# Optimization experiments

Measured on AMD Instinct MI355X. Metric: run time of the kernel, lower is better.

Reference implementation:

```python
import jax, jax.numpy as jnp
import numpy as np
from jax import lax

NEG = -1e30  # log-space 'zero' that stays finite for stable grads

T, B, V, L = 2000, 64, 128, 100


def ctc_cost(acts, labels2d, sizes, label_lens):
    """warp-ctc style CTC: acts are raw logits (T,B,V), blank index 0.
    Returns summed negative log-likelihood over the batch, shape (1,)."""
    Tn, Bn, Vn = acts.shape
    Ln = labels2d.shape[1]
    S = 2 * Ln + 1  # extended label length: blank,l1,blank,l2,...,blank
    lp = jax.nn.log_softmax(acts, axis=-1)  # (T,B,V)

    # extended label sequence per example: even positions blank(0), odd = labels
    ext = jnp.zeros((Bn, S), dtype=labels2d.dtype).at[:, 1::2].set(labels2d)
    # skip (s-2 -> s) allowed iff ext[s] != blank and ext[s] != ext[s-2]
    prev2 = jnp.concatenate([jnp.full((Bn, 2), -1, ext.dtype), ext[:, :-2]], axis=1)
    can_skip = (ext != 0) & (ext != prev2)  # (B,S)

    # gather per-state emission log-probs for all timesteps: (T,B,S)
    lp_ext = jnp.take_along_axis(lp, jnp.broadcast_to(ext[None], (Tn, Bn, S)), axis=2)

    # alpha init at t=0: states 0 (blank) and 1 (first label)
    alpha0 = (jnp.full((Bn, S), NEG, lp.dtype)
              .at[:, 0].set(lp_ext[0, :, 0])
              .at[:, 1].set(lp_ext[0, :, 1]))

    # per-timestep activity mask: freeze alpha once t >= sizes[b]
    active = jnp.arange(1, Tn)[:, None] < sizes[None, :]  # (T-1, B)

    def step(alpha, x):
        lp_t, act = x  # (B,S), (B,)
        a1 = jnp.concatenate([jnp.full((Bn, 1), NEG, alpha.dtype), alpha[:, :-1]], axis=1)
        a2 = jnp.concatenate([jnp.full((Bn, 2), NEG, alpha.dtype), alpha[:, :-2]], axis=1)
        a2 = jnp.where(can_skip, a2, NEG)
        new = jnp.logaddexp(jnp.logaddexp(alpha, a1), a2) + lp_t
        alpha = jnp.where(act[:, None], new, alpha)
        return alpha, None

    alpha, _ = lax.scan(step, alpha0, (lp_ext[1:], active))

    # log-likelihood ends at extended states S_b-1 (final blank) and S_b-2 (final label)
    S_b = 2 * label_lens + 1
    last = jnp.take_along_axis(alpha, (S_b - 1)[:, None], axis=1)[:, 0]
    last2 = jnp.take_along_axis(alpha, (S_b - 2)[:, None], axis=1)[:, 0]
    ll = jnp.logaddexp(last, last2)  # (B,)
    return -jnp.sum(ll)[None]  # shape (1,) like the torch module


def setup_inputs() -> dict:
    key = jax.random.key(0)
    k1, k2, k3 = jax.random.split(key, 3)
    inp = jax.random.normal(k1, (T, B, V), dtype=jnp.float32)
    # labels in [1, V): 0 is reserved for blank
    target = jax.random.randint(k2, (B * L,), 1, V, dtype=jnp.int32)
    # frame counts in [T//2, T], always >= 2L+1 so every path is feasible
    sizes = jax.random.randint(k3, (B,), T // 2, T + 1, dtype=jnp.int32)
    label_lens = jnp.full((B,), L, dtype=jnp.int32)
    return {"input": inp, "target": target, "sizes": sizes, "label_lens": label_lens}


def reference(input, target, sizes, label_lens):
    labels2d = target.reshape(sizes.shape[0], -1)  # all label_lens equal -> clean reshape
    return ctc_cost(input, labels2d, sizes, label_lens)
```

## Files before the change

kernel.cpp:

```cpp
#include <hip/hip_runtime.h>


#define TT 2000
#define BB 64
#define VV 128
#define LL 100
#define RECW 56
#define REC_BASE 256
#define NEGF (-1e30f)
#define L2E 1.44269504f
#define LN2 0.69314718f

__device__ __forceinline__ float wave_max64(float v) {
#pragma unroll
  for (int o = 32; o > 0; o >>= 1) v = fmaxf(v, __shfl_xor(v, o, 64));
  return v;
}
__device__ __forceinline__ float wave_sum64(float v) {
#pragma unroll
  for (int o = 32; o > 0; o >>= 1) v += __shfl_xor(v, o, 64);
  return v;
}
__device__ __forceinline__ float blo(unsigned u) { return __uint_as_float(u << 16); }
__device__ __forceinline__ float bhi(unsigned u) { return __uint_as_float(u & 0xFFFF0000u); }
__device__ __forceinline__ unsigned b16(float x) {
  unsigned b = __float_as_uint(x);
  return (b + 0x7FFFu + ((b >> 16) & 1u)) >> 16;
}

__global__ __launch_bounds__(256) void k_gather(const float* __restrict__ acts,
                                                const int* __restrict__ target,
                                                float* __restrict__ ws) {
  const int lane = threadIdx.x & 63;
  const int w = threadIdx.x >> 6;
  const int r = blockIdx.x * 4 + w;
  if (r >= TT * BB) return;
  const int b = r % BB;
  const int t = r / BB;
  const float* row = acts + (size_t)r * VV;
  float x0 = row[lane];
  float x1 = row[lane + 64];
  float m = wave_max64(fmaxf(x0, x1));
  float e = __builtin_exp2f((x0 - m) * L2E) + __builtin_exp2f((x1 - m) * L2E);
  float s = wave_sum64(e);
  float lse = m + __builtin_log2f(s) * LN2;
  const int* lab = target + b * LL;
  const int j = lane;
  int ilo = (2 * j < 100) ? 2 * j : 99;
  int ihi = (2 * j + 1 < 100) ? 2 * j + 1 : 99;
  int cl = lab[ilo], ch = lab[ihi];
  float ya = __shfl(x0, cl & 63, 64), yb = __shfl(x1, cl & 63, 64);
  float ylo = (cl < 64) ? ya : yb;
  float yc = __shfl(x0, ch & 63, 64), yd = __shfl(x1, ch & 63, 64);
  float yhi = (ch < 64) ? yc : yd;
  float glo = (j < 50) ? (ylo - lse) : NEGF;
  float ghi = (j < 50) ? (yhi - lse) : NEGF;
  float gb = __shfl(x0, 0, 64) - lse;
  float gm = wave_max64(fmaxf(fmaxf(glo, ghi), gb));
  float qlo = __builtin_exp2f((glo - gm) * L2E);
  float qhi = __builtin_exp2f((ghi - gm) * L2E);
  unsigned u = b16(qlo) | (b16(qhi) << 16);
  unsigned* rec = (unsigned*)(ws + REC_BASE + ((size_t)b * TT + t) * RECW);
  if (j < 50) rec[2 + j] = u;
  if (j == 50) rec[52] = 0u;
  if (j == 0) {
    ((float*)rec)[0] = __builtin_exp2f((gb - gm) * L2E);
    ((float*)rec)[1] = gm;
  }
}

#define BPER __builtin_amdgcn_ds_bpermute
#define CL50(x) ((x) < 0 ? 0 : ((x) > 50 ? 50 : (x)))

#define DECLR(P) float2 P##h0, P##h1, P##h2, P##h3; \
                 unsigned P##b0, P##b1, P##b2, P##b3, P##c0, P##c1, P##c2, P##c3, P##uA

#define PREF(P, bidx) do {                                                   \
  int bi_ = (bidx); bi_ = (bi_ < bcap) ? bi_ : bcap; if (bi_ < 0) bi_ = 0;   \
  const float* r0_ = recs_b + (size_t)(tA + TS * 4 * bi_) * RECW;            \
  P##h0 = *(const float2*)(r0_);                                             \
  P##h1 = *(const float2*)(r0_ + TS * RECW);                                 \
  P##h2 = *(const float2*)(r0_ + TS * 2 * RECW);                             \
  P##h3 = *(const float2*)(r0_ + TS * 3 * RECW);                             \
  P##b0 = ((const unsigned*)r0_)[pbofs];                                     \
  P##c0 = ((const unsigned*)r0_)[pcofs];                                     \
  P##b1 = ((const unsigned*)(r0_ + TS * RECW))[pbofs];                       \
  P##c1 = ((const unsigned*)(r0_ + TS * RECW))[pcofs];                       \
  P##b2 = ((const unsigned*)(r0_ + TS * 2 * RECW))[pbofs];                   \
  P##c2 = ((const unsigned*)(r0_ + TS * 2 * RECW))[pcofs];                   \
  P##b3 = ((const unsigned*)(r0_ + TS * 3 * RECW))[pbofs];                   \
  P##c3 = ((const unsigned*)(r0_ + TS * 3 * RECW))[pcofs];                   \
  P##uA = ((const unsigned*)r0_)[payofs];                                    \
} while (0)

#define STEP(qbv, gmv, cx, cy, bx, by, ay, NH) do {                          \
  const float qb_ = (qbv); msum += (gmv);                                    \
  o3 = __builtin_fmaf(cs_o3, o1, o3 + o2) * (cy);                            \
  o2 = (o2 + o1) * qb_;                                                      \
  o1 = __builtin_fmaf(cs_o1, h1, o1 + o0) * (cx);                            \
  o0 = (o0 + h1) * qb_;                                                      \
  if (NH >= 1) { h1 = __builtin_fmaf(cs_h1, h3, h1 + h2) * (by);             \
                 h2 = (h2 + h3) * qb_; }                                     \
  if (NH >= 2) { h3 = __builtin_fmaf(cs_h3, h5, h3 + h4) * (bx);             \
                 h4 = (h4 + h5) * qb_; }                                     \
  if (NH >= 3) { h5 = __builtin_fmaf(cs_h5, h7, h5 + h6) * (ay);             \
                 h6 = (h6 + h7) * qb_; }                                     \
} while (0)

#define UQ(P, K, QV) float4 QV; do {                                         \
  if constexpr (DIR) {                                                       \
    QV = (float4){bhi(P##b##K), blo(P##b##K),                                \
                  bhi(P##c##K) * cmask, blo(P##c##K) * cmask};               \
  } else {                                                                   \
    QV = (float4){blo(P##b##K), bhi(P##b##K), blo(P##c##K), bhi(P##c##K)};   \
  }                                                                          \
} while (0)

#define COMPA(P) do {                                                        \
  UQ(P, 0, q0_); UQ(P, 1, q1_); UQ(P, 2, q2_); UQ(P, 3, q3_);                \
  float aYv = DIR ? blo(P##uA) : bhi(P##uA);                                 \
  STEP(P##h0.x, P##h0.y, q0_.z, q0_.w, q0_.x, q0_.y, aYv, 3);                \
  STEP(P##h1.x, P##h1.y, q1_.z, q1_.w, q1_.x, q1_.y, 0.f, 2);                \
  STEP(P##h2.x, P##h2.y, q2_.z, q2_.w, q2_.x, q2_.y, 0.f, 1);                \
  STEP(P##h3.x, P##h3.y, q3_.z, q3_.w, 0.f, 0.f, 0.f, 0);                    \
  unsigned p01_ = b16(o0) | (b16(o1) << 16);                                 \
  unsigned p23_ = b16(o2) | (b16(o3) << 16);                                 \
  *(uint2*)(exbU + 2 * l) = (uint2){p01_, p23_};                             \
  exbU[128 + l] = (unsigned)offs;                                            \
} while (0)

#define FINL() do {                                                          \
  asm volatile("" ::: "memory");                                             \
  uint2 W1_ = *(const uint2*)(exbU + 2 * ((l >= 1) ? (l - 1) : 0));          \
  uint2 W2_ = *(const uint2*)(exbU + 2 * ((l >= 2) ? (l - 2) : 0));          \
  int ro1_ = (int)exbU[128 + ((l >= 1) ? (l - 1) : 0)];                      \
  int ro2_ = (int)exbU[128 + ((l >= 2) ? (l - 2) : 0)];                      \
  ro1_ = (l >= 1) ? ro1_ : -(1 << 29);                                       \
  ro2_ = (l >= 2) ? ro2_ : -(1 << 29);                                       \
  float m_ = fmaxf(fmaxf(o0, o1), fmaxf(o2, o3));                            \
  int eb_ = (int)((__float_as_uint(m_) >> 23) & 255u);                       \
  int t1_ = offs + (eb_ ? (eb_ - 127) : -126);                               \
  int mx_ = (ro1_ > ro2_) ? ro1_ : ro2_;                                     \
  int onew_ = (t1_ > mx_) ? t1_ : mx_;                                       \
  int ds_ = offs - onew_;  ds_ = (ds_ < -300) ? -300 : ds_;                  \
  int d1_ = ro1_ - onew_, d2_ = ro2_ - onew_;                                \
  d1_ = (d1_ < -300) ? -300 : d1_;                                           \
  d2_ = (d2_ < -300) ? -300 : d2_;                                           \
  o0 = ldexpf(o0, ds_); o1 = ldexpf(o1, ds_);                                \
  o2 = ldexpf(o2, ds_); o3 = ldexpf(o3, ds_);                                \
  h1 = ldexpf(bhi(W1_.y), d1_);                                              \
  h2 = ldexpf(blo(W1_.y), d1_);                                              \
  h3 = ldexpf(bhi(W1_.x), d1_);                                              \
  h4 = ldexpf(blo(W1_.x), d1_);                                              \
  h5 = ldexpf(bhi(W2_.y), d2_);                                              \
  h6 = ldexpf(blo(W2_.y), d2_);                                              \
  h7 = ldexpf(bhi(W2_.x), d2_);                                              \
  offs = onew_;                                                              \
} while (0)

template <int DIR>
__device__ __forceinline__ void run_chain(const int* __restrict__ target,
                                          const int* __restrict__ lablens,
                                          const float* __restrict__ recs_b,
                                          float* exb, int size, int b, int l) {
  unsigned* exbU = (unsigned*)exb;
  const int mid = (size - 1) >> 1;
  const int sizeP = DIR ? (size - 1 - mid) : (mid + 1);
  const int* lab = target + b * LL;
  const int lc = (l < 50) ? l : 50;
  const int tA = DIR ? (size - 2) : 1;
  constexpr int TS = DIR ? -1 : 1;
  const int bcap = DIR ? ((size - 5) >> 2) : 498;
  const int pbofs = 2 + (DIR ? CL50(50 - l) : CL50(l - 1));
  const int pcofs = 2 + (DIR ? CL50(49 - l) : CL50(l));
  const int payofs = 2 + (DIR ? CL50(51 - l) : CL50(l - 2));
  const float cmask = (l < 50) ? 1.f : 0.f;
  const int idx1 = ((l + 63) & 63) << 2;
  const float msk1 = (4 * l - 1 >= 0) ? 1.f : 0.f;
  int i0, i1, i2, i3, i4, i5;
  if constexpr (DIR == 0) { i0 = 2*l+1; i1 = 2*l; i2 = 2*l-1; i3 = 2*l-2; i4 = 2*l-3; i5 = 2*l-4; }
  else { i0 = 98-2*l; i1 = 99-2*l; i2 = 100-2*l; i3 = 101-2*l; i4 = 102-2*l; i5 = 103-2*l; }
#define CLM(x) ((x) < 0 ? 0 : ((x) > 99 ? 99 : (x)))
  const int La = lab[CLM(i0)], Lb_ = lab[CLM(i1)], Lc = lab[CLM(i2)];
  const int Ld = lab[CLM(i3)], Le = lab[CLM(i4)], Lf = lab[CLM(i5)];
  const float cs_o3 = (La != Lb_) ? 1.f : 0.f;
  const float cs_o1 = (Lb_ != Lc) ? 1.f : 0.f;
  const float cs_h1 = (Lc != Ld) ? 1.f : 0.f;
  const float cs_h3 = (Ld != Le) ? 1.f : 0.f;
  const float cs_h5 = (Le != Lf) ? 1.f : 0.f;
  float o0 = 0.f, o1 = 0.f, o2 = 0.f, o3 = 0.f;
  float h1 = 0.f, h2 = 0.f, h3 = 0.f, h4 = 0.f, h5 = 0.f, h6 = 0.f, h7 = 0.f;
  int offs = 0;
  float msum;
  if constexpr (DIR == 0) {
    msum = recs_b[1];
    float q0i = blo(((const unsigned*)recs_b)[2]);
    if (l == 0) { o0 = recs_b[0]; o1 = q0i; }
    if (l == 1) { h3 = q0i; h4 = recs_b[0]; }
    if (l == 2) { h7 = q0i; }
  } else {
    const float* recL = recs_b + (size_t)(size - 1) * RECW;
    msum = recL[1];
    const int Lbv = lablens[b];
    const int r0v = 200 - 2 * Lbv;
    auto gi = [&](int rho) -> float {
      if (rho != r0v && rho != r0v + 1) return 0.f;
      if ((rho & 1) == 0) return recL[0];
      int mm = 99 - ((rho - 1) >> 1);
      unsigned u = ((const unsigned*)recL)[2 + (mm >> 1)];
      return (mm & 1) ? bhi(u) : blo(u);
    };
    o0 = gi(4*l); o1 = gi(4*l+1); o2 = gi(4*l+2); o3 = gi(4*l+3);
    h1 = gi(4*l-1); h2 = gi(4*l-2); h3 = gi(4*l-3); h4 = gi(4*l-4);
    h5 = gi(4*l-5); h6 = gi(4*l-6); h7 = gi(4*l-7);
  }

  const int nb = (sizeP - 1) >> 2;
  DECLR(A); DECLR(B); DECLR(C);
  PREF(A, 0); PREF(B, 1);
  int blk = 0;
  for (; blk + 3 <= nb; blk += 3) {
    COMPA(A); PREF(C, blk + 2); FINL();
    COMPA(B); PREF(A, blk + 3); FINL();
    COMPA(C); PREF(B, blk + 4); FINL();
  }
  if (nb - blk >= 1) { COMPA(A); FINL(); }
  if (nb - blk >= 2) { COMPA(B); FINL(); }
  {
    int rno1 = BPER(idx1, offs);
    int dtl = rno1 - offs;
    dtl = (dtl > 120) ? 120 : ((dtl < -300) ? -300 : dtl);
    for (int tau = 1 + 4 * nb; tau < sizeP; ++tau) {
      const float* rt = recs_b + (size_t)(DIR ? (size - 1 - tau) : tau) * RECW;
      float2 hh = *(const float2*)rt;
      float cx, cy;
      if constexpr (DIR == 0) {
        unsigned u = ((const unsigned*)rt)[2 + lc];
        cx = blo(u); cy = bhi(u);
      } else {
        unsigned u = ((const unsigned*)rt)[2 + CL50(50 - l)];
        cx = bhi(u) * cmask; cy = blo(u) * cmask;
      }
      int rp = BPER(idx1, __float_as_int(o3));
      float p = ldexpf(__int_as_float(rp), dtl) * msk1;
      msum += hh.y;
      o3 = __builtin_fmaf(cs_o3, o1, o3 + o2) * cy;
      o2 = (o2 + o1) * hh.x;
      o1 = __builtin_fmaf(cs_o1, p, o1 + o0) * cx;
      o0 = (o0 + p) * hh.x;
    }
    if constexpr (DIR == 0) {
      int rp = BPER(idx1, __float_as_int(o3));
      float p = ldexpf(__int_as_float(rp), dtl) * msk1;
      o3 = __builtin_fmaf(cs_o3, o1, o3 + o2);
      o2 = o2 + o1;
      o1 = __builtin_fmaf(cs_o1, p, o1 + o0);
      o0 = o0 + p;
    }
  }
  asm volatile("" ::: "memory");
  ((float4*)exb)[l] = (float4){o0, o1, o2, o3};
  ((int*)exb)[256 + l] = offs;
  if (l == 0) exb[320] = msum;
}

__global__ __launch_bounds__(128, 1) void k_alpha(const int* __restrict__ target,
                                                  const int* __restrict__ sizes,
                                                  const int* __restrict__ lablens,
                                                  float* __restrict__ ws) {
  __shared__ float ldsA[2 * 384];
  const int b = blockIdx.x;
  const int dirw = threadIdx.x >> 6;
  const int l = threadIdx.x & 63;
  float* exb = ldsA + dirw * 384;
  const int size = sizes[b];
  const float* recs_b = ws + REC_BASE + (size_t)b * TT * RECW;
  if (dirw == 0) run_chain<0>(target, lablens, recs_b, exb, size, b, l);
  else           run_chain<1>(target, lablens, recs_b, exb, size, b, l);
  __syncthreads();
  if (dirw == 0) {
    const float* fa = ldsA;
    const float* ba = ldsA + 384;
    float4 av = ((const float4*)fa)[l];
    int eF = ((const int*)fa)[256 + l];
    float msF = fa[320], msB = ba[320];
    float pr0, pr1, pr2, pr3; int ex0, ex1, ex2, ex3, sb0, sb1, sb2, sb3;
#define CMP(k, AV, PR, EX, SBE) do {                                         \
      int s_ = 4 * l + (k);                                                  \
      int rho_ = 200 - s_;                                                   \
      int rc_ = (rho_ < 0) ? 0 : rho_;                                       \
      float g_ = ba[rc_];                                                    \
      int eB_ = ((const int*)ba)[256 + (rc_ >> 2)];                          \
      float p_ = (AV) * g_;                                                  \
      bool ok_ = (rho_ >= 0) && (p_ > 0.f);                                  \
      int eb_ = (int)((__float_as_uint(p_) >> 23) & 255u);                   \
      SBE = eF + eB_;                                                        \
      EX = ok_ ? (SBE + (eb_ ? eb_ - 127 : -140)) : (int)0xC0000000;         \
      PR = ok_ ? p_ : 0.f;                                                   \
    } while (0)
    CMP(0, av.x, pr0, ex0, sb0);
    CMP(1, av.y, pr1, ex1, sb1);
    CMP(2, av.z, pr2, ex2, sb2);
    CMP(3, av.w, pr3, ex3, sb3);
    int Em = ex0 > ex1 ? ex0 : ex1;
    Em = ex2 > Em ? ex2 : Em;
    Em = ex3 > Em ? ex3 : Em;
#pragma unroll
    for (int o = 32; o > 0; o >>= 1) {
      int t = __shfl_xor(Em, o, 64);
      Em = (t > Em) ? t : Em;
    }
    float v = 0.f;
#define ACC(PR, SBE) do { if (PR > 0.f) {                                    \
      int sh_ = SBE - Em; sh_ = sh_ < -300 ? -300 : (sh_ > 300 ? 300 : sh_); \
      v += ldexpf(PR, sh_); } } while (0)
    ACC(pr0, sb0); ACC(pr1, sb1); ACC(pr2, sb2); ACC(pr3, sb3);
    float S = wave_sum64(v);
    if (l == 0) ws[b] = msF + msB + LN2 * ((float)Em + __builtin_log2f(S));
  }
}

__global__ __launch_bounds__(64) void k_final(const float* __restrict__ ws, float* __restrict__ out) {
  float v = (threadIdx.x < BB) ? ws[threadIdx.x] : 0.0f;
  v = wave_sum64(v);
  if (threadIdx.x == 0) out[0] = -v;
}

extern "C" void kernel_launch(void* const* d_in, const int* in_sizes, int n_in,
                              void* d_out, int out_size, void* d_ws, size_t ws_size,
                              hipStream_t stream) {
  const float* acts  = (const float*)d_in[0];
  const int* target  = (const int*)d_in[1];
  const int* sizes   = (const int*)d_in[2];
  const int* lablens = (const int*)d_in[3];
  float* ws  = (float*)d_ws;
  float* out = (float*)d_out;
  const int nrec = TT * BB;
  k_gather<<<dim3(nrec / 4), dim3(256), 0, stream>>>(acts, target, ws);
  k_alpha<<<dim3(BB), dim3(128), 0, stream>>>(target, sizes, lablens, ws);
  k_final<<<dim3(1), dim3(64), 0, stream>>>(ws, out);
}
```

Before: 125.2 us.

## Prefetch alpha-chain record blocks via global_load_lds into a 4-slot LDS ring

Replaces the register-based triple prefetch of per-block record data with asynchronous global-to-LDS loads into a four-slot ring buffer, then reads each slot from LDS when its vmcnt wait completes. This is meant to cut VGPR pressure and keep three blocks of loads in flight ahead of the serial recurrence, hiding global memory latency. It adds LDS traffic and explicit vmcnt waits with sched barriers, which could serialize the loop if the wait counts are wrong. The loop unroll also changes from three to two.

Result: slower. 157.8 us (+26.1%).

```diff
diff --git a/kernel.cpp b/kernel.cpp
--- a/kernel.cpp
+++ b/kernel.cpp
@@ -10,6 +10,9 @@
 #define NEGF (-1e30f)
 #define L2E 1.44269504f
 #define LN2 0.69314718f
+
+#define SLOTU 640
+#define WREGU (4 * SLOTU + 384)
 
 __device__ __forceinline__ float wave_max64(float v) {
 #pragma unroll
@@ -69,28 +72,47 @@
   }
 }
 
+__device__ __forceinline__ void gl_lds4(const float* g, float* l) {
+  __builtin_amdgcn_global_load_lds(
+      (const __attribute__((address_space(1))) unsigned int*)g,
+      (__attribute__((address_space(3))) unsigned int*)l, 4, 0, 0);
+}
+#define WAITV(N) do { asm volatile("s_waitcnt vmcnt(" #N ")" ::: "memory");  \
+                      __builtin_amdgcn_sched_barrier(0); } while (0)
 #define BPER __builtin_amdgcn_ds_bpermute
 #define CL50(x) ((x) < 0 ? 0 : ((x) > 50 ? 50 : (x)))
 
 #define DECLR(P) float2 P##h0, P##h1, P##h2, P##h3; \
                  unsigned P##b0, P##b1, P##b2, P##b3, P##c0, P##c1, P##c2, P##c3, P##uA
 
-#define PREF(P, bidx) do {                                                   \
+#define ISSUE(bidx) do {                                                     \
   int bi_ = (bidx); bi_ = (bi_ < bcap) ? bi_ : bcap; if (bi_ < 0) bi_ = 0;   \
+  float* sb_ = slots + (((unsigned)(bidx)) & 3u) * SLOTU;                    \
   const float* r0_ = recs_b + (size_t)(tA + TS * 4 * bi_) * RECW;            \
-  P##h0 = *(const float2*)(r0_);                                             \
-  P##h1 = *(const float2*)(r0_ + TS * RECW);                                 \
-  P##h2 = *(const float2*)(r0_ + TS * 2 * RECW);                             \
-  P##h3 = *(const float2*)(r0_ + TS * 3 * RECW);                             \
-  P##b0 = ((const unsigned*)r0_)[pbofs];                                     \
-  P##c0 = ((const unsigned*)r0_)[pcofs];                                     \
-  P##b1 = ((const unsigned*)(r0_ + TS * RECW))[pbofs];                       \
-  P##c1 = ((const unsigned*)(r0_ + TS * RECW))[pcofs];                       \
-  P##b2 = ((const unsigned*)(r0_ + TS * 2 * RECW))[pbofs];                   \
-  P##c2 = ((const unsigned*)(r0_ + TS * 2 * RECW))[pcofs];                   \
-  P##b3 = ((const unsigned*)(r0_ + TS * 3 * RECW))[pbofs];                   \
-  P##c3 = ((const unsigned*)(r0_ + TS * 3 * RECW))[pcofs];                   \
-  P##uA = ((const unsigned*)r0_)[payofs];                                    \
+  gl_lds4(r0_ + pbofs,                sb_);                                  \
+  gl_lds4(r0_ + TS * RECW + pbofs,    sb_ + 64);                             \
+  gl_lds4(r0_ + TS * 2 * RECW + pbofs, sb_ + 128);                           \
+  gl_lds4(r0_ + TS * 3 * RECW + pbofs, sb_ + 192);                           \
+  gl_lds4(r0_ + pcofs,                sb_ + 256);                            \
+  gl_lds4(r0_ + TS * RECW + pcofs,    sb_ + 320);                            \
+  gl_lds4(r0_ + TS * 2 * RECW + pcofs, sb_ + 384);                           \
+  gl_lds4(r0_ + TS * 3 * RECW + pcofs, sb_ + 448);                           \
+  gl_lds4(r0_ + payofs,               sb_ + 512);                            \
+  gl_lds4(r0_ + hoff,                 sb_ + 576);                            \
+} while (0)
+
+#define LREAD(P, bidx) do {                                                  \
+  const float* sbF_ = slots + (((unsigned)(bidx)) & 3u) * SLOTU;             \
+  const unsigned* sb_ = (const unsigned*)sbF_;                               \
+  P##b0 = sb_[l];        P##b1 = sb_[64 + l];                                \
+  P##b2 = sb_[128 + l];  P##b3 = sb_[192 + l];                               \
+  P##c0 = sb_[256 + l];  P##c1 = sb_[320 + l];                               \
+  P##c2 = sb_[384 + l];  P##c3 = sb_[448 + l];                               \
+  P##uA = sb_[512 + l];                                                      \
+  float4 H01_ = *(const float4*)(sbF_ + 576);                                \
+  float4 H23_ = *(const float4*)(sbF_ + 580);                                \
+  P##h0 = (float2){H01_.x, H01_.y}; P##h1 = (float2){H01_.z, H01_.w};        \
+  P##h2 = (float2){H23_.x, H23_.y}; P##h3 = (float2){H23_.z, H23_.w};        \
 } while (0)
 
 #define STEP(qbv, gmv, cx, cy, bx, by, ay, NH) do {                          \
@@ -162,7 +184,9 @@
 __device__ __forceinline__ void run_chain(const int* __restrict__ target,
                                           const int* __restrict__ lablens,
                                           const float* __restrict__ recs_b,
-                                          float* exb, int size, int b, int l) {
+                                          float* wbase, int size, int b, int l) {
+  float* slots = wbase;
+  float* exb = wbase + 4 * SLOTU;
   unsigned* exbU = (unsigned*)exb;
   const int mid = (size - 1) >> 1;
   const int sizeP = DIR ? (size - 1 - mid) : (mid + 1);
@@ -174,6 +198,7 @@
   const int pbofs = 2 + (DIR ? CL50(50 - l) : CL50(l - 1));
   const int pcofs = 2 + (DIR ? CL50(49 - l) : CL50(l));
   const int payofs = 2 + (DIR ? CL50(51 - l) : CL50(l - 2));
+  const int hoff = (l < 8) ? (TS * (l >> 1) * RECW + (l & 1)) : 0;
   const float cmask = (l < 50) ? 1.f : 0.f;
   const int idx1 = ((l + 63) & 63) << 2;
   const float msk1 = (4 * l - 1 >= 0) ? 1.f : 0.f;
@@ -216,16 +241,17 @@
   }
 
   const int nb = (sizeP - 1) >> 2;
-  DECLR(A); DECLR(B); DECLR(C);
-  PREF(A, 0); PREF(B, 1);
+  DECLR(A); DECLR(B);
+  ISSUE(0); ISSUE(1); ISSUE(2);
+  WAITV(20);
+  LREAD(A, 0);
   int blk = 0;
-  for (; blk + 3 <= nb; blk += 3) {
-    COMPA(A); PREF(C, blk + 2); FINL();
-    COMPA(B); PREF(A, blk + 3); FINL();
-    COMPA(C); PREF(B, blk + 4); FINL();
-  }
-  if (nb - blk >= 1) { COMPA(A); FINL(); }
-  if (nb - blk >= 2) { COMPA(B); FINL(); }
+  for (; blk + 2 <= nb; blk += 2) {
+    COMPA(A); ISSUE(blk + 3); WAITV(20); LREAD(B, blk + 1); FINL();
+    COMPA(B); ISSUE(blk + 4); WAITV(20); LREAD(A, blk + 2); FINL();
+  }
+  if (blk < nb) { COMPA(A); FINL(); }
+  WAITV(0);
   {
     int rno1 = BPER(idx1, offs);
     int dtl = rno1 - offs;
@@ -268,19 +294,19 @@
                                                   const int* __restrict__ sizes,
                                                   const int* __restrict__ lablens,
                                                   float* __restrict__ ws) {
-  __shared__ float ldsA[2 * 384];
+  __shared__ float ldsA[2 * WREGU];
   const int b = blockIdx.x;
   const int dirw = threadIdx.x >> 6;
   const int l = threadIdx.x & 63;
-  float* exb = ldsA + dirw * 384;
+  float* wbase = ldsA + dirw * WREGU;
   const int size = sizes[b];
   const float* recs_b = ws + REC_BASE + (size_t)b * TT * RECW;
-  if (dirw == 0) run_chain<0>(target, lablens, recs_b, exb, size, b, l);
-  else           run_chain<1>(target, lablens, recs_b, exb, size, b, l);
+  if (dirw == 0) run_chain<0>(target, lablens, recs_b, wbase, size, b, l);
+  else           run_chain<1>(target, lablens, recs_b, wbase, size, b, l);
   __syncthreads();
   if (dirw == 0) {
-    const float* fa = ldsA;
-    const float* ba = ldsA + 384;
+    const float* fa = ldsA + 4 * SLOTU;
+    const float* ba = ldsA + WREGU + 4 * SLOTU;
     float4 av = ((const float4*)fa)[l];
     int eF = ((const int*)fa)[256 + l];
     float msF = fa[320], msB = ba[320];
```
